# Optimization experiments

Measured on AMD Instinct MI355X. Metric: run time of the kernel, lower is better.

## Reference

```python
import jax, jax.numpy as jnp
import numpy as np
import math

DIM = 512
WINDOW = 4
TOPK = 8


def setup_inputs() -> dict:
    key = jax.random.key(0)
    ks = jax.random.split(key, 14)
    B, N, D = 4, 4096, DIM
    s = 0.02
    return {
        'mu':  jax.random.normal(ks[0], (B, N, D), jnp.float32),
        'Wq':  jax.random.normal(ks[1], (D, D), jnp.float32) * s,
        'bq':  jnp.zeros((D,), jnp.float32),
        'Wk':  jax.random.normal(ks[2], (D, D), jnp.float32) * s,
        'bk':  jnp.zeros((D,), jnp.float32),
        'Wv':  jax.random.normal(ks[3], (D, D), jnp.float32) * s,
        'bv':  jnp.zeros((D,), jnp.float32),
        'Wm1': jax.random.normal(ks[4], (2 * D, D), jnp.float32) * s,
        'bm1': jnp.zeros((D,), jnp.float32),
        'Wm2': jax.random.normal(ks[5], (D, D), jnp.float32) * s,
        'bm2': jnp.zeros((D,), jnp.float32),
        'Wo':  jax.random.normal(ks[6], (2 * D, D), jnp.float32) * s,
        'bo':  jnp.zeros((D,), jnp.float32),
    }


def reference(mu, Wq, bq, Wk, bk, Wv, bv, Wm1, bm1, Wm2, bm2, Wo, bo):
    B, N, D = mu.shape
    W = WINDOW
    # ---- local windowed message passing ----
    padded = jnp.pad(mu, ((0, 0), (W, 0), (0, 0)))  # left-pad seq with W zeros
    # neighbors[:, n, w-1] = mu[:, n-w] (zeros if n-w < 0); [B, N, W, D]
    neighbors = jnp.stack([padded[:, W - w:W - w + N, :] for w in range(1, W + 1)], axis=2)
    self_exp = jnp.broadcast_to(mu[:, :, None, :], neighbors.shape)
    h = jnp.concatenate([self_exp, neighbors], axis=-1)  # [B, N, W, 2D]
    h = jax.nn.silu(h @ Wm1 + bm1)
    local_msgs = (h @ Wm2 + bm2).mean(axis=2)  # [B, N, D]
    # ---- sparse causal global attention ----
    q = mu @ Wq + bq
    k = mu @ Wk + bk
    v = mu @ Wv + bv
    scores = jnp.einsum('bnd,bmd->bnm', q, k) * (1.0 / math.sqrt(D))
    causal = jnp.tril(jnp.ones((N, N), bool))
    scores = jnp.where(causal, scores, -jnp.inf)
    # top-k then softmax over kept entries == softmax over scatter(-inf elsewhere)
    topk_vals, topk_idx = jax.lax.top_k(scores, TOPK)  # [B, N, K]
    probs = jax.nn.softmax(topk_vals, axis=-1)
    bi = jnp.arange(B)[:, None, None]
    ni = jnp.arange(N)[None, :, None]
    attn = jnp.zeros_like(scores).at[bi, ni, topk_idx].set(probs)  # [B, N, N]
    global_msgs = jnp.einsum('bnm,bmd->bnd', attn, v)
    return jnp.concatenate([local_msgs, global_msgs], axis=-1) @ Wo + bo
```

## Files before the change

kernel.cpp:

```cpp
#include <hip/hip_runtime.h>
#include <math.h>

#define DIM 512
#define NSEQ 4096
#define BATCH 4
#define ROWS (BATCH * NSEQ)

typedef unsigned long long u64;
typedef unsigned int u32;
typedef unsigned short u16;
typedef __attribute__((ext_vector_type(8))) short bf16x8;
typedef __attribute__((ext_vector_type(4))) float f32x4;

__device__ __forceinline__ u32 to_bf16(float f) {
  u32 x = __float_as_uint(f);
  return (x + 0x7fffu + ((x >> 16) & 1u)) >> 16;
}
__device__ __forceinline__ u32 pk2(float a, float b) {
  return to_bf16(a) | (to_bf16(b) << 16);
}
__device__ __forceinline__ uint4 pk8(float4 a, float4 b) {
  return make_uint4(pk2(a.x, a.y), pk2(a.z, a.w), pk2(b.x, b.y), pk2(b.z, b.w));
}

__device__ __forceinline__ void insert_top8(u64 (&a)[8], u64 key) {
  if (key <= a[7]) return;
  a[7] = key;
#pragma unroll
  for (int i = 7; i > 0; --i) {
    u64 x = a[i - 1], y = a[i];
    u64 hi = x > y ? x : y;
    u64 lo = x > y ? y : x;
    a[i - 1] = hi;
    a[i] = lo;
  }
}
template<int NN>
__device__ __forceinline__ void insert_topN(u64 (&a)[NN], u64 key) {
  if (key <= a[NN - 1]) return;
  a[NN - 1] = key;
#pragma unroll
  for (int i = NN - 1; i > 0; --i) {
    u64 x = a[i - 1], y = a[i];
    u64 hi = x > y ? x : y;
    u64 lo = x > y ? y : x;
    a[i - 1] = hi;
    a[i] = lo;
  }
}
__device__ __forceinline__ float decode_val(u64 key) {
  u32 ord = (u32)(key >> 32);
  u32 s = (ord & 0x80000000u) ? (ord ^ 0x80000000u) : ~ord;
  return __uint_as_float(s);
}
__device__ __forceinline__ u64 pack_key(float v, int m) {
  u32 sb = __float_as_uint(v);
  u32 ord = sb ^ ((sb >> 31) ? 0xFFFFFFFFu : 0x80000000u);
  return ((u64)ord << 32) | (u32)(~(u32)m);
}

__device__ __forceinline__ int fbal(int sub) {
  const int g = sub >> 5, i = sub & 31;
  return (g == 0) ? i : (g == 1) ? (63 - i) : (g == 2) ? (64 + i) : (127 - i);
}

__global__ __launch_bounds__(256) void gemm64qk(const float* __restrict__ mu,
                                                const float* __restrict__ Wq,
                                                const float* __restrict__ bq,
                                                const float* __restrict__ Wk,
                                                const float* __restrict__ bk,
                                                float* __restrict__ Q,
                                                float* __restrict__ Kf,
                                                u16* __restrict__ Kc) {
  __shared__ float As[16][68];
  __shared__ float Bs[16][68];
  const int tid = threadIdx.x;
  const int tx = tid & 15, ty = tid >> 4;
  const int bx = blockIdx.x;
  const bool isK = bx >= 8;
  const int n0 = (bx & 7) * 64;
  const int m0 = blockIdx.y * 64;
  const float* W = isK ? Wk : Wq;
  const float* bias = isK ? bk : bq;
  float* C = isK ? Kf : Q;
  const int arow = tid >> 2, ac4 = (tid & 3) * 4;
  const int bkk = tid >> 4, bc4 = (tid & 15) * 4;
  float acc[4][4] = {};
  for (int k0 = 0; k0 < DIM; k0 += 16) {
    float4 a4 = *(const float4*)(mu + (size_t)(m0 + arow) * DIM + (k0 + ac4));
    float4 b4 = *(const float4*)(W + (size_t)(k0 + bkk) * DIM + (n0 + bc4));
    As[ac4 + 0][arow] = a4.x;
    As[ac4 + 1][arow] = a4.y;
    As[ac4 + 2][arow] = a4.z;
    As[ac4 + 3][arow] = a4.w;
    *(float4*)&Bs[bkk][bc4] = b4;
    __syncthreads();
#pragma unroll
    for (int kk = 0; kk < 16; ++kk) {
      float4 av = *(const float4*)&As[kk][ty * 4];
      float4 bv = *(const float4*)&Bs[kk][tx * 4];
#pragma unroll
      for (int i = 0; i < 4; ++i) {
        float a = (i == 0) ? av.x : (i == 1) ? av.y : (i == 2) ? av.z : av.w;
        acc[i][0] = fmaf(a, bv.x, acc[i][0]);
        acc[i][1] = fmaf(a, bv.y, acc[i][1]);
        acc[i][2] = fmaf(a, bv.z, acc[i][2]);
        acc[i][3] = fmaf(a, bv.w, acc[i][3]);
      }
    }
    __syncthreads();
  }
  float4 bb = *(const float4*)(bias + n0 + tx * 4);
#pragma unroll
  for (int i = 0; i < 4; ++i) {
    int row = m0 + ty * 4 + i;
    int col = n0 + tx * 4;
    size_t off = (size_t)row * DIM + col;
    float4 o;
    o.x = acc[i][0] + bb.x;
    o.y = acc[i][1] + bb.y;
    o.z = acc[i][2] + bb.z;
    o.w = acc[i][3] + bb.w;
    *(float4*)(C + off) = o;
    if (isK) {
      int batch = row >> 12, key = row & 4095;
      int kt = key >> 6, kl = key & 63;
      int chunk = col >> 5;
      size_t didx = ((size_t)batch << 21) +
                    ((size_t)((kt * 16 + chunk) * 64 + kl)) * 32 + (col & 31);
      *(uint2*)(Kc + didx) = make_uint2(pk2(o.x, o.y), pk2(o.z, o.w));
    }
  }
}

__global__ __launch_bounds__(256) void wtrans6(const float* __restrict__ Wv,
                                               const float* __restrict__ Wm1,
                                               const float* __restrict__ Wm2,
                                               const float* __restrict__ Wo,
                                               u16* __restrict__ WT) {
  const size_t DD = (size_t)DIM * DIM;
  const int y = blockIdx.y;
  const float* src = (y == 0) ? Wv
                   : (y == 1) ? Wm1
                   : (y == 2) ? Wm1 + DD
                   : (y == 3) ? Wm2
                   : (y == 4) ? Wo
                              : Wo + DD;
  u16* dst = WT + (size_t)y * DD;
  int o = blockIdx.x * 256 + threadIdx.x;
  int n = o >> 7;
  int k0 = (o & 127) * 4;
  float a0 = src[(size_t)(k0 + 0) * DIM + n];
  float a1 = src[(size_t)(k0 + 1) * DIM + n];
  float a2 = src[(size_t)(k0 + 2) * DIM + n];
  float a3 = src[(size_t)(k0 + 3) * DIM + n];
  ((uint2*)dst)[(n << 7) + (k0 >> 2)] = make_uint2(pk2(a0, a1), pk2(a2, a3));
}

__global__ __launch_bounds__(256) void gemmbf(const float* __restrict__ A, int lda,
                                              const u16* __restrict__ WT,
                                              const float* __restrict__ bias,
                                              float* C, int ldc, int accum) {
  __shared__ u16 As[128 * 32];
  __shared__ u16 Bs[128 * 32];
  const int tid = threadIdx.x;
  const int n0 = blockIdx.x * 128;
  const int m0 = blockIdx.y * 128;
  const int l = tid & 63, lr = l & 15, lu = l >> 4;
  const int wid = tid >> 6, wr = wid >> 1, wc = wid & 1;
  const int srow = tid >> 1, shalf = tid & 1;
  f32x4 acc[4][4] = {};
  for (int k0 = 0; k0 < 512; k0 += 32) {
    __syncthreads();
    {
      const float4* a4 = (const float4*)(A + (size_t)(m0 + srow) * lda + k0 + shalf * 16);
      float4 u0 = a4[0], u1 = a4[1], u2 = a4[2], u3 = a4[3];
      int sw = (srow >> 1) & 3;
      *(uint4*)&As[srow * 32 + ((shalf * 2 + 0) ^ sw) * 8] = pk8(u0, u1);
      *(uint4*)&As[srow * 32 + ((shalf * 2 + 1) ^ sw) * 8] = pk8(u2, u3);
    }
    {
      const uint4* b4 = (const uint4*)(WT + (size_t)(n0 + srow) * 512 + k0 + shalf * 16);
      uint4 v0 = b4[0], v1 = b4[1];
      int sw = (srow >> 1) & 3;
      *(uint4*)&Bs[srow * 32 + ((shalf * 2 + 0) ^ sw) * 8] = v0;
      *(uint4*)&Bs[srow * 32 + ((shalf * 2 + 1) ^ sw) * 8] = v1;
    }
    __syncthreads();
    bf16x8 af[4], bf_[4];
#pragma unroll
    for (int fr = 0; fr < 4; ++fr) {
      int row = wr * 64 + fr * 16 + lr;
      af[fr] = *(const bf16x8*)&As[row * 32 + (lu ^ ((row >> 1) & 3)) * 8];
    }
#pragma unroll
    for (int fc = 0; fc < 4; ++fc) {
      int col = wc * 64 + fc * 16 + lr;
      bf_[fc] = *(const bf16x8*)&Bs[col * 32 + (lu ^ ((col >> 1) & 3)) * 8];
    }
#pragma unroll
    for (int fr = 0; fr < 4; ++fr)
#pragma unroll
      for (int fc = 0; fc < 4; ++fc)
        acc[fr][fc] = __builtin_amdgcn_mfma_f32_16x16x32_bf16(af[fr], bf_[fc], acc[fr][fc], 0, 0, 0);
  }
#pragma unroll
  for (int fr = 0; fr < 4; ++fr)
#pragma unroll
    for (int fc = 0; fc < 4; ++fc) {
      int col = n0 + wc * 64 + fc * 16 + lr;
      float bb = bias ? bias[col] : 0.f;
#pragma unroll
      for (int j = 0; j < 4; ++j) {
        int row = m0 + wr * 64 + fr * 16 + lu * 4 + j;
        size_t off = (size_t)row * ldc + col;
        float o = acc[fr][fc][j] + bb;
        if (accum) o += C[off];
        C[off] = o;
      }
    }
}

__global__ __launch_bounds__(256) void silu_combine(const float* P,
                                                    const float* bm1,
                                                    float* Gout) {
  size_t idx = (size_t)blockIdx.x * 256 + threadIdx.x;
  int r = (int)(idx >> 7);
  int c4 = (int)(idx & 127);
  int n = r & (NSEQ - 1);
  const float4* P4 = (const float4*)P;
  float4 a = P4[(size_t)r * 256 + c4];
  float4 bm = ((const float4*)bm1)[c4];
  float bx = a.x + bm.x, by = a.y + bm.y, bz = a.z + bm.z, bw = a.w + bm.w;
  float sx = 0.f, sy = 0.f, sz = 0.f, sw = 0.f;
#pragma unroll
  for (int w = 1; w <= 4; ++w) {
    float ex = bx, ey = by, ez = bz, ew = bw;
    if (n >= w) {
      float4 nb = P4[(size_t)(r - w) * 256 + 128 + c4];
      ex += nb.x; ey += nb.y; ez += nb.z; ew += nb.w;
    }
    sx += ex / (1.f + expf(-ex));
    sy += ey / (1.f + expf(-ey));
    sz += ez / (1.f + expf(-ez));
    sw += ew / (1.f + expf(-ew));
  }
  ((float4*)Gout)[(size_t)r * 128 + c4] =
      make_float4(0.25f * sx, 0.25f * sy, 0.25f * sz, 0.25f * sw);
}

__global__ __launch_bounds__(256, 4) void attn_fused(const float* __restrict__ Qf,
                                                     const float* __restrict__ Kf,
                                                     const u16* __restrict__ Kc,
                                                     const float* __restrict__ V,
                                                     float* __restrict__ G) {
  __shared__ union UA {
    struct { u16 Qs[16 * 512]; u64 cand[256][8]; } s;
    float Qf32[16][512];
  } uA;
  __shared__ int cidx[16][16];
  __shared__ u64 exkey[16][16];
  __shared__ float psm[16][8];
  __shared__ int pidx[16][8];

  const int tid = threadIdx.x;
  const int bid = blockIdx.x;
  const int xcd = bid & 7;
  const int b = xcd >> 1;
  const int par = xcd & 1;
  const int sub = bid >> 3;
  const int qt = 2 * fbal(sub) + par;
  const int n0 = qt * 16;
  const size_t rb = (size_t)b * NSEQ;
  const float SCALE_F = 0.04419417382415922f;

  const int l = tid & 63, lr = l & 15, lu = l >> 4;
  const int wid = tid >> 6;
  const int mbase = lu * 4;

  {
    int row = tid >> 4, part = tid & 15;
    const float4* src = (const float4*)(Qf + ((rb + n0 + row) << 9));
#pragma unroll
    for (int c = 0; c < 4; ++c) {
      int slot = part * 4 + c;
      float4 x = src[slot * 2], y = src[slot * 2 + 1];
      *(uint4*)&uA.s.Qs[row * 512 + (slot ^ (row & 7)) * 8] = pk8(x, y);
    }
  }
  __syncthreads();

  u64 best[8] = {};
  const int nq = n0 + lr;

  const int nkt = (n0 + 16 + 63) >> 6;
  const int lo = (lr * 32) + lu * 8;
  for (int kt = wid; kt < nkt; kt += 4) {
    const int m0 = kt << 6;
    const u16* kb = Kc + ((size_t)b << 21) + (size_t)kt * 32768;
    f32x4 acc[4] = {};
    bf16x8 kcur[4], knxt[4];
#pragma unroll
    for (int fk = 0; fk < 4; ++fk)
      kcur[fk] = *(const bf16x8*)(kb + fk * 512 + lo);
#pragma unroll
    for (int ks = 0; ks < 16; ++ks) {
      if (ks < 15) {
        const u16* cb = kb + (ks + 1) * 2048;
#pragma unroll
        for (int fk = 0; fk < 4; ++fk)
          knxt[fk] = *(const bf16x8*)(cb + fk * 512 + lo);
      }
      bf16x8 qf = *(const bf16x8*)&uA.s.Qs[lr * 512 + ((ks * 4 + lu) ^ (lr & 7)) * 8];
#pragma unroll
      for (int fk = 0; fk < 4; ++fk)
        acc[fk] = __builtin_amdgcn_mfma_f32_16x16x32_bf16(kcur[fk], qf, acc[fk], 0, 0, 0);
      if (ks < 15) {
#pragma unroll
        for (int fk = 0; fk < 4; ++fk) kcur[fk] = knxt[fk];
      }
    }
    if (m0 + 63 <= n0) {
#pragma unroll
      for (int fk = 0; fk < 4; ++fk)
#pragma unroll
        for (int j = 0; j < 4; ++j)
          insert_top8(best, pack_key(acc[fk][j], m0 + fk * 16 + mbase + j));
    } else {
#pragma unroll
      for (int fk = 0; fk < 4; ++fk)
#pragma unroll
        for (int j = 0; j < 4; ++j) {
          int m = m0 + fk * 16 + mbase + j;
          if (m <= nq) insert_top8(best, pack_key(acc[fk][j], m));
        }
    }
  }

  __syncthreads();
#pragma unroll
  for (int i = 0; i < 8; ++i) uA.s.cand[tid][i] = best[i];
  __syncthreads();

  if (tid < 16) {
    u64 mb[16] = {};
    for (int w = 0; w < 4; ++w)
      for (int u = 0; u < 4; ++u) {
        const u64* cl = uA.s.cand[w * 64 + u * 16 + tid];
#pragma unroll
        for (int i = 0; i < 8; ++i) insert_topN<16>(mb, cl[i]);
      }
#pragma unroll
    for (int i = 0; i < 16; ++i)
      cidx[tid][i] = (mb[i] != 0ULL) ? (int)(~(u32)mb[i]) : -1;
  }
  __syncthreads();

  {
    int row = tid >> 4, seg = tid & 15;
    const float4* src = (const float4*)(Qf + ((rb + n0 + row) << 9));
    float4* dst = (float4*)&uA.Qf32[row][0];
#pragma unroll
    for (int c = 0; c < 8; ++c) dst[seg * 8 + c] = src[seg * 8 + c];
  }
  __syncthreads();

  {
    const int g = tid >> 2;
    const int lsub = tid & 3;
    const int qi = g >> 2;
    const int cblk = g & 3;
    const float4* q4 = (const float4*)&uA.Qf32[qi][0];
#pragma unroll
    for (int cc = 0; cc < 4; ++cc) {
      int c = cblk * 4 + cc;
      int ci = cidx[qi][c];
      float4 p = make_float4(0.f, 0.f, 0.f, 0.f);
      if (ci >= 0) {
        const float4* k4 = (const float4*)(Kf + ((rb + ci) << 9));
#pragma unroll 8
        for (int t = 0; t < 32; ++t) {
          float4 kv = k4[4 * t + lsub];
          float4 qv = q4[4 * t + lsub];
          p.x = fmaf(kv.x, qv.x, p.x);
          p.y = fmaf(kv.y, qv.y, p.y);
          p.z = fmaf(kv.z, qv.z, p.z);
          p.w = fmaf(kv.w, qv.w, p.w);
        }
      }
      p.x += __shfl_xor(p.x, 2);
      p.y += __shfl_xor(p.y, 2);
      p.z += __shfl_xor(p.z, 2);
      p.w += __shfl_xor(p.w, 2);
      p.x += __shfl_xor(p.x, 1);
      p.y += __shfl_xor(p.y, 1);
      p.z += __shfl_xor(p.z, 1);
      p.w += __shfl_xor(p.w, 1);
      float rx = p.x + p.z;
      float ry = p.y + p.w;
      float r = rx + ry;
      if (lsub == 0)
        exkey[qi][c] = (ci >= 0) ? pack_key(r * SCALE_F, ci) : 0ULL;
    }
  }
  __syncthreads();

  if (tid < 16) {
    u64 mb[8] = {};
#pragma unroll
    for (int t2 = 0; t2 < 16; ++t2) insert_top8(mb, exkey[tid][t2]);
    float vmax = decode_val(mb[0]);
    float e[8];
#pragma unroll
    for (int i = 0; i < 8; ++i)
      e[i] = (mb[i] != 0ULL) ? expf(decode_val(mb[i]) - vmax) : 0.f;
    float s01 = e[0] + e[1], s23 = e[2] + e[3];
    float s45 = e[4] + e[5], s67 = e[6] + e[7];
    float ssum = (s01 + s23) + (s45 + s67);
#pragma unroll
    for (int i = 0; i < 8; ++i) {
      psm[tid][i] = e[i] / ssum;
      pidx[tid][i] = (mb[i] != 0ULL) ? (int)(~(u32)mb[i]) : 0;
    }
  }
  __syncthreads();

  {
    const int qi = tid >> 4, seg = tid & 15;
    float pp[8];
    int ix[8];
#pragma unroll
    for (int i = 0; i < 8; ++i) { pp[i] = psm[qi][i]; ix[i] = pidx[qi][i]; }
    const float4* V4 = (const float4*)V;
    float4* G4 = (float4*)G;
    const size_t ob = ((rb + n0 + qi) << 7) + seg * 8;
#pragma unroll
    for (int it = 0; it < 8; ++it) {
      float4 a = make_float4(0.f, 0.f, 0.f, 0.f);
#pragma unroll
      for (int i = 0; i < 8; ++i) {
        float4 vv = V4[((rb + ix[i]) << 7) + seg * 8 + it];
        a.x = fmaf(pp[i], vv.x, a.x);
        a.y = fmaf(pp[i], vv.y, a.y);
        a.z = fmaf(pp[i], vv.z, a.z);
        a.w = fmaf(pp[i], vv.w, a.w);
      }
      G4[ob + it] = a;
    }
  }
}

extern "C" void kernel_launch(void* const* d_in, const int* in_sizes, int n_in,
                              void* d_out, int out_size, void* d_ws, size_t ws_size,
                              hipStream_t stream) {
  const float* mu = (const float*)d_in[0];
  const float* Wq = (const float*)d_in[1];
  const float* bq = (const float*)d_in[2];
  const float* Wk = (const float*)d_in[3];
  const float* bk = (const float*)d_in[4];
  const float* Wv = (const float*)d_in[5];
  const float* bv = (const float*)d_in[6];
  const float* Wm1 = (const float*)d_in[7];
  const float* bm1 = (const float*)d_in[8];
  const float* Wm2 = (const float*)d_in[9];
  const float* bm2 = (const float*)d_in[10];
  const float* Wo = (const float*)d_in[11];
  const float* bo = (const float*)d_in[12];
  float* out = (float*)d_out;

  float* ws = (float*)d_ws;
  const size_t RD = (size_t)ROWS * DIM;
  const size_t DD = (size_t)DIM * DIM;
  float* X1 = ws;
  float* X2 = X1 + RD;
  float* X3 = X2 + RD;
  float* X4 = X3 + RD;
  u16* Kc = (u16*)(X4 + RD);
  u16* WT = Kc + RD;
  u16* WvT = WT;
  u16* Wm1aT = WT + DD;
  u16* Wm2T = WT + 3 * DD;
  u16* WoTT = WT + 4 * DD;
  u16* WoBT = WT + 5 * DD;

  dim3 blk(256);
  dim3 gqk(16, ROWS / 64);
  dim3 gbf(DIM / 128, ROWS / 128);
  dim3 gbf2(2 * DIM / 128, ROWS / 128);

  wtrans6<<<dim3(256, 6), blk, 0, stream>>>(Wv, Wm1, Wm2, Wo, WT);

  gemm64qk<<<gqk, blk, 0, stream>>>(mu, Wq, bq, Wk, bk, X1, X2, Kc);

  gemmbf<<<gbf, blk, 0, stream>>>(mu, 512, WvT, bv, X3, 512, 0);

  attn_fused<<<dim3(1024), blk, 0, stream>>>(X1, X2, Kc, X3, X4);

  gemmbf<<<gbf2, blk, 0, stream>>>(mu, 512, Wm1aT, (const float*)nullptr, X1, 1024, 0);
  silu_combine<<<dim3(ROWS * 128 / 256), blk, 0, stream>>>(X1, bm1, X3);
  gemmbf<<<gbf, blk, 0, stream>>>(X3, 512, Wm2T, bm2, X1, 512, 0);

  gemmbf<<<gbf, blk, 0, stream>>>(X1, 512, WoTT, bo, out, 512, 0);
  gemmbf<<<gbf, blk, 0, stream>>>(X4, 512, WoBT, (const float*)nullptr, out, 512, 1);
}
```

Measured before the change: 755.8 us.

## Process 32 queries per attention block and enlarge QK projection tiles

The fused attention kernel now runs 512 threads per block. Each block handles two 16-query groups that share every bf16 K fragment load, so K tile traffic per query is halved. The candidate merge and exact fp32 rescoring stages are repeated for each group, and the block load-balancing map is simplified. Separately, the Q/K projection GEMM moves from 64x64 tiles with 4x4 per thread to 128x128 tiles with 8x8 per thread, raising arithmetic intensity. The risks are higher register pressure under launch_bounds(512,4), which could cause spills, and fewer blocks for load balancing.

```diff
diff --git a/kernel.cpp b/kernel.cpp
--- a/kernel.cpp
+++ b/kernel.cpp
@@ -57,11 +57,6 @@
   u32 sb = __float_as_uint(v);
   u32 ord = sb ^ ((sb >> 31) ? 0xFFFFFFFFu : 0x80000000u);
   return ((u64)ord << 32) | (u32)(~(u32)m);
-}
-
-__device__ __forceinline__ int fbal(int sub) {
-  const int g = sub >> 5, i = sub & 31;
-  return (g == 0) ? i : (g == 1) ? (63 - i) : (g == 2) ? (64 + i) : (127 - i);
 }
 
 __global__ __launch_bounds__(256) void gemm64qk(const float* __restrict__ mu,
@@ -72,63 +67,71 @@
                                                 float* __restrict__ Q,
                                                 float* __restrict__ Kf,
                                                 u16* __restrict__ Kc) {
-  __shared__ float As[16][68];
-  __shared__ float Bs[16][68];
+  __shared__ float As[16][132];
+  __shared__ float Bs[16][132];
   const int tid = threadIdx.x;
   const int tx = tid & 15, ty = tid >> 4;
   const int bx = blockIdx.x;
-  const bool isK = bx >= 8;
-  const int n0 = (bx & 7) * 64;
-  const int m0 = blockIdx.y * 64;
+  const bool isK = bx >= 4;
+  const int n0 = (bx & 3) * 128;
+  const int m0 = blockIdx.y * 128;
   const float* W = isK ? Wk : Wq;
   const float* bias = isK ? bk : bq;
   float* C = isK ? Kf : Q;
-  const int arow = tid >> 2, ac4 = (tid & 3) * 4;
-  const int bkk = tid >> 4, bc4 = (tid & 15) * 4;
-  float acc[4][4] = {};
+  const int arow = tid >> 1, ah8 = (tid & 1) * 8;
+  const int bkk = tid >> 4, bc8 = (tid & 15) * 8;
+  float acc[8][8] = {};
   for (int k0 = 0; k0 < DIM; k0 += 16) {
-    float4 a4 = *(const float4*)(mu + (size_t)(m0 + arow) * DIM + (k0 + ac4));
-    float4 b4 = *(const float4*)(W + (size_t)(k0 + bkk) * DIM + (n0 + bc4));
-    As[ac4 + 0][arow] = a4.x;
-    As[ac4 + 1][arow] = a4.y;
-    As[ac4 + 2][arow] = a4.z;
-    As[ac4 + 3][arow] = a4.w;
-    *(float4*)&Bs[bkk][bc4] = b4;
+    float4 a0 = *(const float4*)(mu + (size_t)(m0 + arow) * DIM + (k0 + ah8));
+    float4 a1 = *(const float4*)(mu + (size_t)(m0 + arow) * DIM + (k0 + ah8 + 4));
+    float4 b0 = *(const float4*)(W + (size_t)(k0 + bkk) * DIM + (n0 + bc8));
+    float4 b1 = *(const float4*)(W + (size_t)(k0 + bkk) * DIM + (n0 + bc8 + 4));
+    As[ah8 + 0][arow] = a0.x; As[ah8 + 1][arow] = a0.y;
+    As[ah8 + 2][arow] = a0.z; As[ah8 + 3][arow] = a0.w;
+    As[ah8 + 4][arow] = a1.x; As[ah8 + 5][arow] = a1.y;
+    As[ah8 + 6][arow] = a1.z; As[ah8 + 7][arow] = a1.w;
+    *(float4*)&Bs[bkk][bc8] = b0;
+    *(float4*)&Bs[bkk][bc8 + 4] = b1;
     __syncthreads();
 #pragma unroll
     for (int kk = 0; kk < 16; ++kk) {
-      float4 av = *(const float4*)&As[kk][ty * 4];
-      float4 bv = *(const float4*)&Bs[kk][tx * 4];
-#pragma unroll
-      for (int i = 0; i < 4; ++i) {
-        float a = (i == 0) ? av.x : (i == 1) ? av.y : (i == 2) ? av.z : av.w;
-        acc[i][0] = fmaf(a, bv.x, acc[i][0]);
-        acc[i][1] = fmaf(a, bv.y, acc[i][1]);
-        acc[i][2] = fmaf(a, bv.z, acc[i][2]);
-        acc[i][3] = fmaf(a, bv.w, acc[i][3]);
-      }
+      float4 av0 = *(const float4*)&As[kk][ty * 8];
+      float4 av1 = *(const float4*)&As[kk][ty * 8 + 4];
+      float4 bv0 = *(const float4*)&Bs[kk][tx * 8];
+      float4 bv1 = *(const float4*)&Bs[kk][tx * 8 + 4];
+      float a8[8] = {av0.x, av0.y, av0.z, av0.w, av1.x, av1.y, av1.z, av1.w};
+      float b8[8] = {bv0.x, bv0.y, bv0.z, bv0.w, bv1.x, bv1.y, bv1.z, bv1.w};
+#pragma unroll
+      for (int i = 0; i < 8; ++i)
+#pragma unroll
+        for (int j = 0; j < 8; ++j)
+          acc[i][j] = fmaf(a8[i], b8[j], acc[i][j]);
     }
     __syncthreads();
   }
-  float4 bb = *(const float4*)(bias + n0 + tx * 4);
-#pragma unroll
-  for (int i = 0; i < 4; ++i) {
-    int row = m0 + ty * 4 + i;
-    int col = n0 + tx * 4;
-    size_t off = (size_t)row * DIM + col;
-    float4 o;
-    o.x = acc[i][0] + bb.x;
-    o.y = acc[i][1] + bb.y;
-    o.z = acc[i][2] + bb.z;
-    o.w = acc[i][3] + bb.w;
-    *(float4*)(C + off) = o;
-    if (isK) {
-      int batch = row >> 12, key = row & 4095;
-      int kt = key >> 6, kl = key & 63;
-      int chunk = col >> 5;
-      size_t didx = ((size_t)batch << 21) +
-                    ((size_t)((kt * 16 + chunk) * 64 + kl)) * 32 + (col & 31);
-      *(uint2*)(Kc + didx) = make_uint2(pk2(o.x, o.y), pk2(o.z, o.w));
+  float4 bb0 = *(const float4*)(bias + n0 + tx * 8);
+  float4 bb1 = *(const float4*)(bias + n0 + tx * 8 + 4);
+#pragma unroll
+  for (int i = 0; i < 8; ++i) {
+    int row = m0 + ty * 8 + i;
+#pragma unroll
+    for (int jb = 0; jb < 2; ++jb) {
+      int col = n0 + tx * 8 + jb * 4;
+      float4 bb = jb ? bb1 : bb0;
+      float4 o;
+      o.x = acc[i][jb * 4 + 0] + bb.x;
+      o.y = acc[i][jb * 4 + 1] + bb.y;
+      o.z = acc[i][jb * 4 + 2] + bb.z;
+      o.w = acc[i][jb * 4 + 3] + bb.w;
+      *(float4*)(C + (size_t)row * DIM + col) = o;
+      if (isK) {
+        int batch = row >> 12, key = row & 4095;
+        int kt = key >> 6, kl = key & 63;
+        int chunk = col >> 5;
+        size_t didx = ((size_t)batch << 21) +
+                      ((size_t)((kt * 16 + chunk) * 64 + kl)) * 32 + (col & 31);
+        *(uint2*)(Kc + didx) = make_uint2(pk2(o.x, o.y), pk2(o.z, o.w));
+      }
     }
   }
 }
@@ -249,28 +252,30 @@
       make_float4(0.25f * sx, 0.25f * sy, 0.25f * sz, 0.25f * sw);
 }
 
-__global__ __launch_bounds__(256, 4) void attn_fused(const float* __restrict__ Qf,
+__global__ __launch_bounds__(512, 4) void attn_fused(const float* __restrict__ Qf,
                                                      const float* __restrict__ Kf,
                                                      const u16* __restrict__ Kc,
                                                      const float* __restrict__ V,
                                                      float* __restrict__ G) {
   __shared__ union UA {
-    struct { u16 Qs[16 * 512]; u64 cand[256][8]; } s;
+    struct { u16 Qs[32 * 512]; u64 cand[512][8]; } s;
     float Qf32[16][512];
   } uA;
-  __shared__ int cidx[16][16];
-  __shared__ u64 exkey[16][16];
-  __shared__ float psm[16][8];
-  __shared__ int pidx[16][8];
+  __shared__ int cidx[32][16];
+  __shared__ u64 exkey[32][16];
+  __shared__ float psm[32][8];
+  __shared__ int pidx[32][8];
 
   const int tid = threadIdx.x;
   const int bid = blockIdx.x;
   const int xcd = bid & 7;
   const int b = xcd >> 1;
   const int par = xcd & 1;
-  const int sub = bid >> 3;
-  const int qt = 2 * fbal(sub) + par;
-  const int n0 = qt * 16;
+  const int rest = bid >> 3;
+  const int f2 = (rest < 32) ? rest : (95 - rest);
+  const int pair = 2 * f2 + par;
+  const int n0 = pair * 32;
+  const int nA = n0 + 15;
   const size_t rb = (size_t)b * NSEQ;
   const float SCALE_F = 0.04419417382415922f;
 
@@ -290,15 +295,17 @@
   }
   __syncthreads();
 
-  u64 best[8] = {};
-  const int nq = n0 + lr;
-
-  const int nkt = (n0 + 16 + 63) >> 6;
+  u64 bestA[8] = {}, bestB[8] = {};
+  const int nqA = n0 + lr;
+  const int nqB = n0 + 16 + lr;
+  const int rowB = 16 + lr;
+
+  const int nkt = (n0 + 32 + 63) >> 6;
   const int lo = (lr * 32) + lu * 8;
-  for (int kt = wid; kt < nkt; kt += 4) {
+  for (int kt = wid; kt < nkt; kt += 8) {
     const int m0 = kt << 6;
     const u16* kb = Kc + ((size_t)b << 21) + (size_t)kt * 32768;
-    f32x4 acc[4] = {};
+    f32x4 accA[4] = {}, accB[4] = {};
     bf16x8 kcur[4], knxt[4];
 #pragma unroll
     for (int fk = 0; fk < 4; ++fk)
@@ -311,40 +318,59 @@
         for (int fk = 0; fk < 4; ++fk)
           knxt[fk] = *(const bf16x8*)(cb + fk * 512 + lo);
       }
-      bf16x8 qf = *(const bf16x8*)&uA.s.Qs[lr * 512 + ((ks * 4 + lu) ^ (lr & 7)) * 8];
+      bf16x8 qfA = *(const bf16x8*)&uA.s.Qs[lr * 512 + ((ks * 4 + lu) ^ (lr & 7)) * 8];
+      bf16x8 qfB = *(const bf16x8*)&uA.s.Qs[rowB * 512 + ((ks * 4 + lu) ^ (rowB & 7)) * 8];
+#pragma unroll
+      for (int fk = 0; fk < 4; ++fk) {
+        accA[fk] = __builtin_amdgcn_mfma_f32_16x16x32_bf16(kcur[fk], qfA, accA[fk], 0, 0, 0);
+        accB[fk] = __builtin_amdgcn_mfma_f32_16x16x32_bf16(kcur[fk], qfB, accB[fk], 0, 0, 0);
+      }
+      if (ks < 15) {
+#pragma unroll
+        for (int fk = 0; fk < 4; ++fk) kcur[fk] = knxt[fk];
+      }
+    }
+    if (m0 <= nA) {
+      if (m0 + 63 <= n0) {
+#pragma unroll
+        for (int fk = 0; fk < 4; ++fk)
+#pragma unroll
+          for (int j = 0; j < 4; ++j)
+            insert_top8(bestA, pack_key(accA[fk][j], m0 + fk * 16 + mbase + j));
+      } else {
+#pragma unroll
+        for (int fk = 0; fk < 4; ++fk)
+#pragma unroll
+          for (int j = 0; j < 4; ++j) {
+            int m = m0 + fk * 16 + mbase + j;
+            if (m <= nqA) insert_top8(bestA, pack_key(accA[fk][j], m));
+          }
+      }
+    }
+    if (m0 + 63 <= n0 + 16) {
 #pragma unroll
       for (int fk = 0; fk < 4; ++fk)
-        acc[fk] = __builtin_amdgcn_mfma_f32_16x16x32_bf16(kcur[fk], qf, acc[fk], 0, 0, 0);
-      if (ks < 15) {
-#pragma unroll
-        for (int fk = 0; fk < 4; ++fk) kcur[fk] = knxt[fk];
-      }
-    }
-    if (m0 + 63 <= n0) {
-#pragma unroll
-      for (int fk = 0; fk < 4; ++fk)
 #pragma unroll
         for (int j = 0; j < 4; ++j)
-          insert_top8(best, pack_key(acc[fk][j], m0 + fk * 16 + mbase + j));
+          insert_top8(bestB, pack_key(accB[fk][j], m0 + fk * 16 + mbase + j));
     } else {
 #pragma unroll
       for (int fk = 0; fk < 4; ++fk)
 #pragma unroll
         for (int j = 0; j < 4; ++j) {
           int m = m0 + fk * 16 + mbase + j;
-          if (m <= nq) insert_top8(best, pack_key(acc[fk][j], m));
+          if (m <= nqB) insert_top8(bestB, pack_key(accB[fk][j], m));
         }
     }
   }
 
   __syncthreads();
 #pragma unroll
-  for (int i = 0; i < 8; ++i) uA.s.cand[tid][i] = best[i];
-  __syncthreads();
-
+  for (int i = 0; i < 8; ++i) uA.s.cand[tid][i] = bestA[i];
+  __syncthreads();
   if (tid < 16) {
     u64 mb[16] = {};
-    for (int w = 0; w < 4; ++w)
+    for (int w = 0; w < 8; ++w)
       for (int u = 0; u < 4; ++u) {
         const u64* cl = uA.s.cand[w * 64 + u * 16 + tid];
 #pragma unroll
@@ -355,57 +381,75 @@
       cidx[tid][i] = (mb[i] != 0ULL) ? (int)(~(u32)mb[i]) : -1;
   }
   __syncthreads();
-
-  {
-    int row = tid >> 4, seg = tid & 15;
-    const float4* src = (const float4*)(Qf + ((rb + n0 + row) << 9));
-    float4* dst = (float4*)&uA.Qf32[row][0];
-#pragma unroll
-    for (int c = 0; c < 8; ++c) dst[seg * 8 + c] = src[seg * 8 + c];
-  }
-  __syncthreads();
-
-  {
-    const int g = tid >> 2;
-    const int lsub = tid & 3;
-    const int qi = g >> 2;
-    const int cblk = g & 3;
-    const float4* q4 = (const float4*)&uA.Qf32[qi][0];
-#pragma unroll
-    for (int cc = 0; cc < 4; ++cc) {
-      int c = cblk * 4 + cc;
-      int ci = cidx[qi][c];
-      float4 p = make_float4(0.f, 0.f, 0.f, 0.f);
-      if (ci >= 0) {
-        const float4* k4 = (const float4*)(Kf + ((rb + ci) << 9));
+#pragma unroll
+  for (int i = 0; i < 8; ++i) uA.s.cand[tid][i] = bestB[i];
+  __syncthreads();
+  if (tid < 16) {
+    u64 mb[16] = {};
+    for (int w = 0; w < 8; ++w)
+      for (int u = 0; u < 4; ++u) {
+        const u64* cl = uA.s.cand[w * 64 + u * 16 + tid];
+#pragma unroll
+        for (int i = 0; i < 8; ++i) insert_topN<16>(mb, cl[i]);
+      }
+#pragma unroll
+    for (int i = 0; i < 16; ++i)
+      cidx[16 + tid][i] = (mb[i] != 0ULL) ? (int)(~(u32)mb[i]) : -1;
+  }
+  __syncthreads();
+
+#pragma unroll
+  for (int grp = 0; grp < 2; ++grp) {
+    {
+      int row = tid >> 5, seg = tid & 31;
+      const float4* src = (const float4*)(Qf + ((rb + n0 + grp * 16 + row) << 9));
+      float4* dst = (float4*)&uA.Qf32[row][0];
+#pragma unroll
+      for (int c = 0; c < 4; ++c) dst[seg * 4 + c] = src[seg * 4 + c];
+    }
+    __syncthreads();
+    {
+      const int g = tid >> 2;
+      const int lsub = tid & 3;
+      const int qi = g >> 3;
+      const int cblk = g & 7;
+      const float4* q4 = (const float4*)&uA.Qf32[qi][0];
+#pragma unroll
+      for (int cc = 0; cc < 2; ++cc) {
+        int c = cblk * 2 + cc;
+        int ci = cidx[grp * 16 + qi][c];
+        float4 p = make_float4(0.f, 0.f, 0.f, 0.f);
+        if (ci >= 0) {
+          const float4* k4 = (const float4*)(Kf + ((rb + ci) << 9));
 #pragma unroll 8
-        for (int t = 0; t < 32; ++t) {
-          float4 kv = k4[4 * t + lsub];
-          float4 qv = q4[4 * t + lsub];
-          p.x = fmaf(kv.x, qv.x, p.x);
-          p.y = fmaf(kv.y, qv.y, p.y);
-          p.z = fmaf(kv.z, qv.z, p.z);
-          p.w = fmaf(kv.w, qv.w, p.w);
+          for (int t = 0; t < 32; ++t) {
+            float4 kv = k4[4 * t + lsub];
+            float4 qv = q4[4 * t + lsub];
+            p.x = fmaf(kv.x, qv.x, p.x);
+            p.y = fmaf(kv.y, qv.y, p.y);
+            p.z = fmaf(kv.z, qv.z, p.z);
+            p.w = fmaf(kv.w, qv.w, p.w);
+          }
         }
-      }
-      p.x += __shfl_xor(p.x, 2);
-      p.y += __shfl_xor(p.y, 2);
-      p.z += __shfl_xor(p.z, 2);
-      p.w += __shfl_xor(p.w, 2);
-      p.x += __shfl_xor(p.x, 1);
-      p.y += __shfl_xor(p.y, 1);
-      p.z += __shfl_xor(p.z, 1);
-      p.w += __shfl_xor(p.w, 1);
-      float rx = p.x + p.z;
-      float ry = p.y + p.w;
-      float r = rx + ry;
-      if (lsub == 0)
-        exkey[qi][c] = (ci >= 0) ? pack_key(r * SCALE_F, ci) : 0ULL;
-    }
-  }
-  __syncthreads();
-
-  if (tid < 16) {
+        p.x += __shfl_xor(p.x, 2);
+        p.y += __shfl_xor(p.y, 2);
+        p.z += __shfl_xor(p.z, 2);
+        p.w += __shfl_xor(p.w, 2);
+        p.x += __shfl_xor(p.x, 1);
+        p.y += __shfl_xor(p.y, 1);
+        p.z += __shfl_xor(p.z, 1);
+        p.w += __shfl_xor(p.w, 1);
+        float rx = p.x + p.z;
+        float ry = p.y + p.w;
+        float r = rx + ry;
+        if (lsub == 0)
+          exkey[grp * 16 + qi][c] = (ci >= 0) ? pack_key(r * SCALE_F, ci) : 0ULL;
+      }
+    }
+    __syncthreads();
+  }
+
+  if (tid < 32) {
     u64 mb[8] = {};
 #pragma unroll
     for (int t2 = 0; t2 < 16; ++t2) insert_top8(mb, exkey[tid][t2]);
@@ -484,7 +528,7 @@
   u16* WoBT = WT + 5 * DD;
 
   dim3 blk(256);
-  dim3 gqk(16, ROWS / 64);
+  dim3 gqk(8, ROWS / 128);
   dim3 gbf(DIM / 128, ROWS / 128);
   dim3 gbf2(2 * DIM / 128, ROWS / 128);
 
@@ -494,7 +538,7 @@
 
   gemmbf<<<gbf, blk, 0, stream>>>(mu, 512, WvT, bv, X3, 512, 0);
 
-  attn_fused<<<dim3(1024), blk, 0, stream>>>(X1, X2, Kc, X3, X4);
+  attn_fused<<<dim3(512), dim3(512), 0, stream>>>(X1, X2, Kc, X3, X4);
 
   gemmbf<<<gbf2, blk, 0, stream>>>(mu, 512, Wm1aT, (const float*)nullptr, X1, 1024, 0);
   silu_combine<<<dim3(ROWS * 128 / 256), blk, 0, stream>>>(X1, bm1, X3);
```

After: 904.8 us. +19.7%, slower.

## Fold Wm2 into Wo weights and enlarge QK GEMM tiles to 128x128

Applied to the files above, without the earlier changes.

Precomputes the product Wm2·Wo_top and a combined bias so the local-message path needs one GEMM instead of two, removing a full ROWSx512x512 GEMM and its intermediate buffer round-trip. It also grows the fp32 Q/K projection kernel's tile from 64x64 to 128x128 with an 8x8 register micro-tile, raising arithmetic intensity. The weight fold adds small per-call setup kernels and an extra bf16 rounding of the combined weights, which may change numerics slightly. The larger per-thread tile raises register pressure and lowers the block count.

```diff
diff --git a/kernel.cpp b/kernel.cpp
--- a/kernel.cpp
+++ b/kernel.cpp
@@ -72,63 +72,71 @@
                                                 float* __restrict__ Q,
                                                 float* __restrict__ Kf,
                                                 u16* __restrict__ Kc) {
-  __shared__ float As[16][68];
-  __shared__ float Bs[16][68];
+  __shared__ float As[16][132];
+  __shared__ float Bs[16][132];
   const int tid = threadIdx.x;
   const int tx = tid & 15, ty = tid >> 4;
   const int bx = blockIdx.x;
-  const bool isK = bx >= 8;
-  const int n0 = (bx & 7) * 64;
-  const int m0 = blockIdx.y * 64;
+  const bool isK = bx >= 4;
+  const int n0 = (bx & 3) * 128;
+  const int m0 = blockIdx.y * 128;
   const float* W = isK ? Wk : Wq;
   const float* bias = isK ? bk : bq;
   float* C = isK ? Kf : Q;
-  const int arow = tid >> 2, ac4 = (tid & 3) * 4;
-  const int bkk = tid >> 4, bc4 = (tid & 15) * 4;
-  float acc[4][4] = {};
+  const int arow = tid >> 1, ah8 = (tid & 1) * 8;
+  const int bkk = tid >> 4, bc8 = (tid & 15) * 8;
+  float acc[8][8] = {};
   for (int k0 = 0; k0 < DIM; k0 += 16) {
-    float4 a4 = *(const float4*)(mu + (size_t)(m0 + arow) * DIM + (k0 + ac4));
-    float4 b4 = *(const float4*)(W + (size_t)(k0 + bkk) * DIM + (n0 + bc4));
-    As[ac4 + 0][arow] = a4.x;
-    As[ac4 + 1][arow] = a4.y;
-    As[ac4 + 2][arow] = a4.z;
-    As[ac4 + 3][arow] = a4.w;
-    *(float4*)&Bs[bkk][bc4] = b4;
+    float4 a0 = *(const float4*)(mu + (size_t)(m0 + arow) * DIM + (k0 + ah8));
+    float4 a1 = *(const float4*)(mu + (size_t)(m0 + arow) * DIM + (k0 + ah8 + 4));
+    float4 b0 = *(const float4*)(W + (size_t)(k0 + bkk) * DIM + (n0 + bc8));
+    float4 b1 = *(const float4*)(W + (size_t)(k0 + bkk) * DIM + (n0 + bc8 + 4));
+    As[ah8 + 0][arow] = a0.x; As[ah8 + 1][arow] = a0.y;
+    As[ah8 + 2][arow] = a0.z; As[ah8 + 3][arow] = a0.w;
+    As[ah8 + 4][arow] = a1.x; As[ah8 + 5][arow] = a1.y;
+    As[ah8 + 6][arow] = a1.z; As[ah8 + 7][arow] = a1.w;
+    *(float4*)&Bs[bkk][bc8] = b0;
+    *(float4*)&Bs[bkk][bc8 + 4] = b1;
     __syncthreads();
 #pragma unroll
     for (int kk = 0; kk < 16; ++kk) {
-      float4 av = *(const float4*)&As[kk][ty * 4];
-      float4 bv = *(const float4*)&Bs[kk][tx * 4];
-#pragma unroll
-      for (int i = 0; i < 4; ++i) {
-        float a = (i == 0) ? av.x : (i == 1) ? av.y : (i == 2) ? av.z : av.w;
-        acc[i][0] = fmaf(a, bv.x, acc[i][0]);
-        acc[i][1] = fmaf(a, bv.y, acc[i][1]);
-        acc[i][2] = fmaf(a, bv.z, acc[i][2]);
-        acc[i][3] = fmaf(a, bv.w, acc[i][3]);
-      }
+      float4 av0 = *(const float4*)&As[kk][ty * 8];
+      float4 av1 = *(const float4*)&As[kk][ty * 8 + 4];
+      float4 bv0 = *(const float4*)&Bs[kk][tx * 8];
+      float4 bv1 = *(const float4*)&Bs[kk][tx * 8 + 4];
+      float a8[8] = {av0.x, av0.y, av0.z, av0.w, av1.x, av1.y, av1.z, av1.w};
+      float b8[8] = {bv0.x, bv0.y, bv0.z, bv0.w, bv1.x, bv1.y, bv1.z, bv1.w};
+#pragma unroll
+      for (int i = 0; i < 8; ++i)
+#pragma unroll
+        for (int j = 0; j < 8; ++j)
+          acc[i][j] = fmaf(a8[i], b8[j], acc[i][j]);
     }
     __syncthreads();
   }
-  float4 bb = *(const float4*)(bias + n0 + tx * 4);
-#pragma unroll
-  for (int i = 0; i < 4; ++i) {
-    int row = m0 + ty * 4 + i;
-    int col = n0 + tx * 4;
-    size_t off = (size_t)row * DIM + col;
-    float4 o;
-    o.x = acc[i][0] + bb.x;
-    o.y = acc[i][1] + bb.y;
-    o.z = acc[i][2] + bb.z;
-    o.w = acc[i][3] + bb.w;
-    *(float4*)(C + off) = o;
-    if (isK) {
-      int batch = row >> 12, key = row & 4095;
-      int kt = key >> 6, kl = key & 63;
-      int chunk = col >> 5;
-      size_t didx = ((size_t)batch << 21) +
-                    ((size_t)((kt * 16 + chunk) * 64 + kl)) * 32 + (col & 31);
-      *(uint2*)(Kc + didx) = make_uint2(pk2(o.x, o.y), pk2(o.z, o.w));
+  float4 bb0 = *(const float4*)(bias + n0 + tx * 8);
+  float4 bb1 = *(const float4*)(bias + n0 + tx * 8 + 4);
+#pragma unroll
+  for (int i = 0; i < 8; ++i) {
+    int row = m0 + ty * 8 + i;
+#pragma unroll
+    for (int jb = 0; jb < 2; ++jb) {
+      int col = n0 + tx * 8 + jb * 4;
+      float4 bb = jb ? bb1 : bb0;
+      float4 o;
+      o.x = acc[i][jb * 4 + 0] + bb.x;
+      o.y = acc[i][jb * 4 + 1] + bb.y;
+      o.z = acc[i][jb * 4 + 2] + bb.z;
+      o.w = acc[i][jb * 4 + 3] + bb.w;
+      *(float4*)(C + (size_t)row * DIM + col) = o;
+      if (isK) {
+        int batch = row >> 12, key = row & 4095;
+        int kt = key >> 6, kl = key & 63;
+        int chunk = col >> 5;
+        size_t didx = ((size_t)batch << 21) +
+                      ((size_t)((kt * 16 + chunk) * 64 + kl)) * 32 + (col & 31);
+        *(uint2*)(Kc + didx) = make_uint2(pk2(o.x, o.y), pk2(o.z, o.w));
+      }
     }
   }
 }
@@ -157,6 +165,27 @@
   ((uint2*)dst)[(n << 7) + (k0 >> 2)] = make_uint2(pk2(a0, a1), pk2(a2, a3));
 }
 
+__global__ __launch_bounds__(256) void wtrans1(const float* __restrict__ src,
+                                               u16* __restrict__ dst) {
+  int o = blockIdx.x * 256 + threadIdx.x;
+  int n = o >> 7;
+  int k0 = (o & 127) * 4;
+  float a0 = src[(size_t)(k0 + 0) * DIM + n];
+  float a1 = src[(size_t)(k0 + 1) * DIM + n];
+  float a2 = src[(size_t)(k0 + 2) * DIM + n];
+  float a3 = src[(size_t)(k0 + 3) * DIM + n];
+  ((uint2*)dst)[(n << 7) + (k0 >> 2)] = make_uint2(pk2(a0, a1), pk2(a2, a3));
+}
+
+__global__ void bcomb_k(const float* __restrict__ bm2, const float* __restrict__ Wo,
+                        const float* __restrict__ bo, float* __restrict__ bc) {
+  int c = blockIdx.x * 256 + threadIdx.x;
+  if (c >= DIM) return;
+  float s = bo[c];
+  for (int k = 0; k < DIM; ++k) s = fmaf(bm2[k], Wo[(size_t)k * DIM + c], s);
+  bc[c] = s;
+}
+
 __global__ __launch_bounds__(256) void gemmbf(const float* __restrict__ A, int lda,
                                               const u16* __restrict__ WT,
                                               const float* __restrict__ bias,
@@ -479,17 +508,23 @@
   u16* WT = Kc + RD;
   u16* WvT = WT;
   u16* Wm1aT = WT + DD;
-  u16* Wm2T = WT + 3 * DD;
   u16* WoTT = WT + 4 * DD;
   u16* WoBT = WT + 5 * DD;
+  float* Wcombf = (float*)(WT + 6 * DD);
+  u16* WcombT = (u16*)(Wcombf + DD);
+  float* bcomb = (float*)(WcombT + DD);
 
   dim3 blk(256);
-  dim3 gqk(16, ROWS / 64);
+  dim3 gqk(8, ROWS / 128);
   dim3 gbf(DIM / 128, ROWS / 128);
   dim3 gbf2(2 * DIM / 128, ROWS / 128);
 
   wtrans6<<<dim3(256, 6), blk, 0, stream>>>(Wv, Wm1, Wm2, Wo, WT);
 
+  gemmbf<<<dim3(4, 4), blk, 0, stream>>>(Wm2, 512, WoTT, (const float*)nullptr, Wcombf, 512, 0);
+  bcomb_k<<<dim3(2), blk, 0, stream>>>(bm2, Wo, bo, bcomb);
+  wtrans1<<<dim3(256), blk, 0, stream>>>(Wcombf, WcombT);
+
   gemm64qk<<<gqk, blk, 0, stream>>>(mu, Wq, bq, Wk, bk, X1, X2, Kc);
 
   gemmbf<<<gbf, blk, 0, stream>>>(mu, 512, WvT, bv, X3, 512, 0);
@@ -498,8 +533,7 @@
 
   gemmbf<<<gbf2, blk, 0, stream>>>(mu, 512, Wm1aT, (const float*)nullptr, X1, 1024, 0);
   silu_combine<<<dim3(ROWS * 128 / 256), blk, 0, stream>>>(X1, bm1, X3);
-  gemmbf<<<gbf, blk, 0, stream>>>(X3, 512, Wm2T, bm2, X1, 512, 0);
-
-  gemmbf<<<gbf, blk, 0, stream>>>(X1, 512, WoTT, bo, out, 512, 0);
+
+  gemmbf<<<gbf, blk, 0, stream>>>(X3, 512, WcombT, bcomb, out, 512, 0);
   gemmbf<<<gbf, blk, 0, stream>>>(X4, 512, WoBT, (const float*)nullptr, out, 512, 1);
 }
```

After: 741.3 us. Within noise of the previous version (-1.9%).
